# Performance work log

Hardware: AMD Instinct MI355X
Metric: run time of the kernel (lower is better)

The kernel has to match this reference:

```python
import jax, jax.numpy as jnp
import numpy as np

NQ = 20          # qubits
NLAYERS = 2
OUT_DIM = 512    # gen_output_dim (= zdim)
COND_DIM = 1
QOUT = min(NQ, OUT_DIM)  # = 20
BATCH = 262144


def _apply_ry(state, theta, w):
    # state: (2,)*NQ real tensor; RY = [[c,-s],[s,c]], c=cos(th/2), s=sin(th/2)
    c = jnp.cos(theta * 0.5)
    s = jnp.sin(theta * 0.5)
    st = jnp.moveaxis(state, w, 0)
    a0, a1 = st[0], st[1]
    st = jnp.stack([c * a0 - s * a1, s * a0 + c * a1])
    return jnp.moveaxis(st, 0, w)


def _apply_cz(state, w):
    # CZ on wires (w, w+1): flip sign where both bits are 1
    st = jnp.moveaxis(state, (w, w + 1), (0, 1))
    st = st.at[1, 1].multiply(-1.0)
    return jnp.moveaxis(st, (0, 1), (w, w + 1))


def _simulate(params):
    # Exact statevector simulation; all gates are real so state stays real.
    state = jnp.zeros((2,) * NQ, dtype=params.dtype).at[(0,) * NQ].set(1.0)
    for layer in range(NLAYERS):
        for w in range(NQ):
            state = _apply_ry(state, params[layer, w], w)
        for w in range(NQ - 1):
            state = _apply_cz(state, w)
    probs = state * state  # (2,)*NQ
    outs = []
    for w in range(QOUT):
        p = jnp.moveaxis(probs, w, 0).reshape(2, -1).sum(axis=1)
        outs.append(p[0] - p[1])  # <Z_w> = P(0) - P(1)
    return jnp.stack(outs)  # (QOUT,)


def setup_inputs() -> dict:
    key = jax.random.key(0)
    k1, k2, k3, k4 = jax.random.split(key, 4)
    cond_batch = jax.random.normal(k1, (BATCH, COND_DIM), dtype=jnp.float32)
    params = 0.05 * jax.random.normal(k2, (NLAYERS, NQ), dtype=jnp.float32)
    fan_in = QOUT + COND_DIM
    bound = 1.0 / np.sqrt(fan_in)
    W = jax.random.uniform(k3, (OUT_DIM, fan_in), jnp.float32, -bound, bound)
    b = jax.random.uniform(k4, (OUT_DIM,), jnp.float32, -bound, bound)
    return {"cond_batch": cond_batch, "params": params, "W": W, "b": b}


def reference(cond_batch, params, W, b):
    # The original qnode ignores `cond`, so the circuit output is identical
    # for every sample in the batch: compute once, broadcast.
    qout = _simulate(params)  # (QOUT,)
    outs = jnp.broadcast_to(qout, (cond_batch.shape[0], QOUT))
    x = jnp.concatenate([outs, cond_batch], axis=1)  # (B, QOUT+COND_DIM)
    return jnp.tanh(x @ W.T + b)  # (B, OUT_DIM)
```

## Files before the change

### kernel.cpp

```cpp
#include <hip/hip_runtime.h>
#include <math.h>

#define NQ 20
#define OUT_DIM 512
#define FAN_IN 21
#define BATCH 262144
#define GRID 2048

typedef float vfloat4 __attribute__((ext_vector_type(4)));

__global__ __launch_bounds__(256)
void fused_kernel(const float* __restrict__ cond,
                  const float* __restrict__ params,
                  const float* __restrict__ W,
                  const float* __restrict__ b,
                  float* __restrict__ out)
{
    __shared__ float qout[NQ];
    __shared__ float sc[128];

    const int t = threadIdx.x;
    const int blk = blockIdx.x;

    if (t < 128) sc[t] = cond[blk * 128 + t];
    if (t < NQ) {
        float p0 = params[t];
        float p1 = params[NQ + t];
        float cl = (t > 0)      ? cosf(params[t - 1]) : 1.0f;
        float cr = (t < NQ - 1) ? cosf(params[t + 1]) : 1.0f;
        qout[t] = cosf(p0) * cosf(p1) - sinf(p0) * sinf(p1) * cl * cr;
    }
    __syncthreads();

    const int half = t >> 7;
    const int j    = (t & 127) << 2;

    vfloat4 A, B;
#pragma unroll
    for (int r = 0; r < 4; ++r) {
        const float* wr = W + (j + r) * FAN_IN;
        float acc = b[j + r];
#pragma unroll
        for (int k = 0; k < NQ; ++k) acc += qout[k] * wr[k];
        B[r] = 2.0f * acc;
        A[r] = 2.0f * wr[NQ];
    }

    float* p = out + (size_t)(blk * 128 + half) * OUT_DIM + j;

#pragma unroll 8
    for (int r = 0; r < 64; ++r) {
        const float c = sc[2 * r + half];
        vfloat4 o;
#pragma unroll
        for (int q = 0; q < 4; ++q) {
            float e = __expf(fmaf(c, A[q], B[q]));
            o[q] = fmaf(-2.0f, __frcp_rn(e + 1.0f), 1.0f);
        }
        *reinterpret_cast<vfloat4*>(p) = o;
        p += 2 * OUT_DIM;
    }
}

extern "C" void kernel_launch(void* const* d_in, const int* in_sizes, int n_in,
                              void* d_out, int out_size, void* d_ws, size_t ws_size,
                              hipStream_t stream)
{
    const float* cond   = (const float*)d_in[0];
    const float* params = (const float*)d_in[1];
    const float* W      = (const float*)d_in[2];
    const float* b      = (const float*)d_in[3];
    float* out = (float*)d_out;

    fused_kernel<<<GRID, 256, 0, stream>>>(cond, params, W, b, out);
}
```

Before: 111.5 us.

## Split per-column coefficient precompute into prep kernel and use raw exp2/rcp

Moves the circuit expectation and per-column linear coefficients into a single-block prep kernel that writes scaled A/B vectors to workspace, so each of the main blocks no longer recomputes trig values and 20-term dot products. The main kernel loads the precomputed coefficients as vectors, folds 2*log2(e) into them, and uses the hardware exp2 and approximate reciprocal builtins in place of __expf and __frcp_rn. This adds a second kernel launch and a dependency between the two kernels, and the approximate reciprocal may slightly change precision.

```diff
diff --git a/kernel.cpp b/kernel.cpp
--- a/kernel.cpp
+++ b/kernel.cpp
@@ -9,42 +9,50 @@
 
 typedef float vfloat4 __attribute__((ext_vector_type(4)));
 
-__global__ __launch_bounds__(256)
-void fused_kernel(const float* __restrict__ cond,
-                  const float* __restrict__ params,
-                  const float* __restrict__ W,
-                  const float* __restrict__ b,
-                  float* __restrict__ out)
+__global__ __launch_bounds__(OUT_DIM)
+void prep_kernel(const float* __restrict__ params,
+                 const float* __restrict__ W,
+                 const float* __restrict__ b,
+                 float* __restrict__ A2,
+                 float* __restrict__ B2)
 {
     __shared__ float qout[NQ];
-    __shared__ float sc[128];
-
-    const int t = threadIdx.x;
-    const int blk = blockIdx.x;
-
-    if (t < 128) sc[t] = cond[blk * 128 + t];
-    if (t < NQ) {
-        float p0 = params[t];
-        float p1 = params[NQ + t];
-        float cl = (t > 0)      ? cosf(params[t - 1]) : 1.0f;
-        float cr = (t < NQ - 1) ? cosf(params[t + 1]) : 1.0f;
-        qout[t] = cosf(p0) * cosf(p1) - sinf(p0) * sinf(p1) * cl * cr;
+    const int j = threadIdx.x;
+    if (j < NQ) {
+        float p0 = params[j];
+        float p1 = params[NQ + j];
+        float cl = (j > 0)      ? cosf(params[j - 1]) : 1.0f;
+        float cr = (j < NQ - 1) ? cosf(params[j + 1]) : 1.0f;
+        qout[j] = cosf(p0) * cosf(p1) - sinf(p0) * sinf(p1) * cl * cr;
     }
     __syncthreads();
 
+    const float TWO_LOG2E = 2.8853900817779268f;
+    const float* wr = W + j * FAN_IN;
+    float acc = b[j];
+#pragma unroll
+    for (int k = 0; k < NQ; ++k) acc += qout[k] * wr[k];
+    B2[j] = TWO_LOG2E * acc;
+    A2[j] = TWO_LOG2E * wr[NQ];
+}
+
+__global__ __launch_bounds__(256)
+void main_kernel(const float* __restrict__ cond,
+                 const float* __restrict__ A2,
+                 const float* __restrict__ B2,
+                 float* __restrict__ out)
+{
+    __shared__ float sc[128];
+    const int t   = threadIdx.x;
+    const int blk = blockIdx.x;
     const int half = t >> 7;
     const int j    = (t & 127) << 2;
 
-    vfloat4 A, B;
-#pragma unroll
-    for (int r = 0; r < 4; ++r) {
-        const float* wr = W + (j + r) * FAN_IN;
-        float acc = b[j + r];
-#pragma unroll
-        for (int k = 0; k < NQ; ++k) acc += qout[k] * wr[k];
-        B[r] = 2.0f * acc;
-        A[r] = 2.0f * wr[NQ];
-    }
+    if (t < 128) sc[t] = cond[blk * 128 + t];
+
+    const vfloat4 A = *reinterpret_cast<const vfloat4*>(A2 + j);
+    const vfloat4 B = *reinterpret_cast<const vfloat4*>(B2 + j);
+    __syncthreads();
 
     float* p = out + (size_t)(blk * 128 + half) * OUT_DIM + j;
 
@@ -54,8 +62,8 @@
         vfloat4 o;
 #pragma unroll
         for (int q = 0; q < 4; ++q) {
-            float e = __expf(fmaf(c, A[q], B[q]));
-            o[q] = fmaf(-2.0f, __frcp_rn(e + 1.0f), 1.0f);
+            float e = __builtin_amdgcn_exp2f(fmaf(c, A[q], B[q]));
+            o[q] = fmaf(-2.0f, __builtin_amdgcn_rcpf(e + 1.0f), 1.0f);
         }
         *reinterpret_cast<vfloat4*>(p) = o;
         p += 2 * OUT_DIM;
@@ -72,5 +80,9 @@
     const float* b      = (const float*)d_in[3];
     float* out = (float*)d_out;
 
-    fused_kernel<<<GRID, 256, 0, stream>>>(cond, params, W, b, out);
+    float* A2 = (float*)d_ws;
+    float* B2 = A2 + OUT_DIM;
+
+    prep_kernel<<<1, OUT_DIM, 0, stream>>>(params, W, b, A2, B2);
+    main_kernel<<<GRID, 256, 0, stream>>>(cond, A2, B2, out);
 }
```

Measured after the change: 102.7 us. -7.9%, faster.
